# Kernel tuning notes

Measured on AMD Instinct MI355X. Metric: run time of the kernel, lower is better.

Reference implementation:

```python
import jax, jax.numpy as jnp
import numpy as np

TEMPERATURE = 0.07
BASE_TEMPERATURE = 0.07
L_MAX = 16  # max number of session labels per dialogue
NEG_INF = -1e30


def setup_inputs() -> dict:
    key = jax.random.key(0)
    k1, k2, k3 = jax.random.split(key, 3)
    B, T, H = 128, 1024, 256
    features = jax.random.normal(k1, (B, T, H), dtype=jnp.float32)
    dialogue_lengths = jax.random.randint(k2, (B,), 1, T + 1)
    labels = jax.random.randint(k3, (B, T), 0, L_MAX)
    return {"features": features, "dialogue_lengths": dialogue_lengths, "labels": labels}


def reference(features, dialogue_lengths, labels):
    B, T, H = features.shape
    valid = jnp.arange(T)[None, :] < dialogue_lengths[:, None]            # [B,T]
    # one-hot label assignment, zeroed at padded positions
    oh = (labels[..., None] == jnp.arange(L_MAX)[None, None, :]) & valid[..., None]
    ohf = oh.astype(features.dtype)                                       # [B,T,L]
    counts = ohf.sum(axis=1)                                              # [B,L]
    # per-dialogue, per-label prototype = mean of member features
    proto_sum = jnp.einsum('btl,bth->blh', ohf, features)                 # [B,L,H]
    prototypes = proto_sum / jnp.maximum(counts, 1.0)[..., None]          # [B,L,H]
    # anchor-vs-prototype logits
    logits = jnp.einsum('bth,blh->btl', features, prototypes) / TEMPERATURE
    present = counts > 0                                                  # [B,L]
    logits = jnp.where(present[:, None, :], logits, NEG_INF)
    log_prob = jax.nn.log_softmax(logits, axis=-1)                        # [B,T,L]
    # mask is one-hot on each token's own label -> mean_log_prob_pos is log_prob at own label
    pos = jnp.take_along_axis(log_prob, labels[..., None], axis=-1)[..., 0]  # [B,T]
    tok_loss = -(TEMPERATURE / BASE_TEMPERATURE) * pos
    per_dialogue = jnp.sum(jnp.where(valid, tok_loss, 0.0), axis=1) / dialogue_lengths.astype(features.dtype)
    return per_dialogue.mean()
```

## Files before the change

### kernel.cpp

```cpp
#include <hip/hip_runtime.h>
#include <math.h>

#define B 128
#define T 1024
#define H 256
#define L 16
#define INV_TEMP (1.0f/0.07f)
#define NEG_INF -1e30f


__global__ __launch_bounds__(256) void proto_kernel(
    const float* __restrict__ feat, const int* __restrict__ dlen,
    const int* __restrict__ labels, float* __restrict__ ws_pp,
    int* __restrict__ ws_cntp, float* __restrict__ out) {
  __shared__ int idx[L][256];
  __shared__ int cnt[L];

  const int bx = blockIdx.x;
  if (bx == 0 && threadIdx.x == 0) out[0] = 0.f;

  const int b = bx >> 4;
  const int seg = (bx >> 2) & 3;
  const int ch = bx & 3;
  const int tid = threadIdx.x;

  const int len = dlen[b];
  if (seg * 256 >= len) return;
  int segLen = len - seg * 256;
  if (segLen > 256) segLen = 256;

  if (tid < L) cnt[tid] = 0;
  __syncthreads();
  if (tid < segLen) {
    const int l = labels[(size_t)b * T + seg * 256 + tid];
    const int p = atomicAdd(&cnt[l], 1);
    idx[l][p] = tid;
  }
  __syncthreads();

  const int l = tid >> 4;
  const int cs = tid & 15;
  const float4* fb4 = (const float4*)feat +
      ((size_t)b * T + seg * 256) * (H / 4) + ch * 16 + cs;

  const int c = cnt[l];
  float4 a = make_float4(0.f, 0.f, 0.f, 0.f);
  int i = 0;
  for (; i + 8 <= c; i += 8) {
    int t8[8];
#pragma unroll
    for (int u = 0; u < 8; ++u) t8[u] = idx[l][i + u];
    float4 f8[8];
#pragma unroll
    for (int u = 0; u < 8; ++u) f8[u] = fb4[(size_t)t8[u] * (H / 4)];
#pragma unroll
    for (int u = 0; u < 8; ++u) {
      a.x += f8[u].x; a.y += f8[u].y; a.z += f8[u].z; a.w += f8[u].w;
    }
  }
  for (; i < c; ++i) {
    const float4 f = fb4[(size_t)idx[l][i] * (H / 4)];
    a.x += f.x; a.y += f.y; a.z += f.z; a.w += f.w;
  }

  *(float4*)(ws_pp + (((size_t)b * 4 + seg) * L + l) * H + ch * 64 + cs * 4) = a;
  if (ch == 0 && tid < L) ws_cntp[(b * 4 + seg) * L + tid] = cnt[tid];
}

__global__ __launch_bounds__(256) void dotsloss_kernel(
    const float* __restrict__ feat, const int* __restrict__ dlen,
    const int* __restrict__ labels, const float* __restrict__ ws_pp,
    const int* __restrict__ ws_cntp, float* __restrict__ out) {
  __shared__ float pr[L * H];
  __shared__ float part[256][L];
  __shared__ int cnts[L];
  __shared__ float red[256];

  const int b = blockIdx.x >> 2;
  const int q = blockIdx.x & 3;
  const int tid = threadIdx.x;

  const int len = dlen[b];
  if (q * 256 >= len) return;
  const int nseg = (len + 255) >> 8;

  if (tid < L) {
    const int* cp = ws_cntp + b * 4 * L + tid;
    int c = 0;
    for (int s = 0; s < nseg; ++s) c += cp[s * L];
    cnts[tid] = c;
  }
  __syncthreads();

  const float4* gp4 = (const float4*)(ws_pp + (size_t)b * 4 * L * H);
  for (int i = tid; i < L * H / 4; i += 256) {
    const int l = i >> 6;
    float4 s = gp4[i];
    for (int sg = 1; sg < nseg; ++sg) {
      const float4 t2 = gp4[sg * (L * 64) + i];
      s.x += t2.x; s.y += t2.y; s.z += t2.z; s.w += t2.w;
    }
    const int cn = cnts[l];
    const float inv = (cn > 0) ? 1.f / (float)cn : 0.f;
    ((float4*)pr)[i] = make_float4(s.x * inv, s.y * inv, s.z * inv, s.w * inv);
  }
  __syncthreads();

  const int ts = tid & 127;
  const int hh = tid >> 7;
  const int t0 = q * 256 + ts;
  const int t1 = t0 + 128;

  const float4* fA = (const float4*)feat + ((size_t)b * T + t0) * (H / 4) + hh * 32;
  const float4* fB = (const float4*)feat + ((size_t)b * T + t1) * (H / 4) + hh * 32;

  float dot0[L], dot1[L];
#pragma unroll
  for (int l = 0; l < L; ++l) { dot0[l] = 0.f; dot1[l] = 0.f; }

#pragma unroll 2
  for (int cb = 0; cb < 8; ++cb) {
    float4 fa[4], fb_[4];
#pragma unroll
    for (int q4 = 0; q4 < 4; ++q4) {
      fa[q4] = fA[cb * 4 + q4];
      fb_[q4] = fB[cb * 4 + q4];
    }
#pragma unroll
    for (int q4 = 0; q4 < 4; ++q4) {
#pragma unroll
      for (int l = 0; l < L; ++l) {
        const float4 p = *(const float4*)&pr[l * H + hh * 128 + cb * 16 + q4 * 4];
        dot0[l] += fa[q4].x * p.x + fa[q4].y * p.y +
                   fa[q4].z * p.z + fa[q4].w * p.w;
        dot1[l] += fb_[q4].x * p.x + fb_[q4].y * p.y +
                   fb_[q4].z * p.z + fb_[q4].w * p.w;
      }
    }
  }

  if (hh == 1) {
#pragma unroll
    for (int l = 0; l < L; ++l) {
      part[ts][l] = dot0[l];
      part[ts + 128][l] = dot1[l];
    }
  }
  __syncthreads();

  float tok = 0.f;
  if (hh == 0) {
#pragma unroll
    for (int k = 0; k < 2; ++k) {
      const int t = t0 + k * 128;
      if (t < len) {
        float lg[L];
#pragma unroll
        for (int l = 0; l < L; ++l) {
          const float d = (k == 0 ? dot0[l] : dot1[l]) + part[ts + k * 128][l];
          lg[l] = (cnts[l] > 0) ? d * INV_TEMP : NEG_INF;
        }
        float m = lg[0];
#pragma unroll
        for (int l = 1; l < L; ++l) m = fmaxf(m, lg[l]);
        float se = 0.f;
#pragma unroll
        for (int l = 0; l < L; ++l) se += expf(lg[l] - m);
        const float lsp = m + logf(se);

        const int lab = labels[(size_t)b * T + t];
        float pos = 0.f;
#pragma unroll
        for (int l = 0; l < L; ++l) pos += (l == lab) ? lg[l] : 0.f;

        tok += lsp - pos;
      }
    }
  }

  red[tid] = tok;
  __syncthreads();
#pragma unroll
  for (int s = 128; s > 0; s >>= 1) {
    if (tid < s) red[tid] += red[tid + s];
    __syncthreads();
  }
  if (tid == 0) atomicAdd(out, red[0] / ((float)len * (float)B));
}

extern "C" void kernel_launch(void* const* d_in, const int* in_sizes, int n_in,
                              void* d_out, int out_size, void* d_ws, size_t ws_size,
                              hipStream_t stream) {
  const float* feat = (const float*)d_in[0];
  const int* dlen = (const int*)d_in[1];
  const int* labels = (const int*)d_in[2];
  float* out = (float*)d_out;

  float* ws_pp = (float*)d_ws;
  int* ws_cntp = (int*)(ws_pp + (size_t)B * 4 * L * H);

  proto_kernel<<<B * 16, 256, 0, stream>>>(feat, dlen, labels, ws_pp,
                                           ws_cntp, out);
  dotsloss_kernel<<<B * 4, 256, 0, stream>>>(feat, dlen, labels, ws_pp,
                                             ws_cntp, out);
}
```

Baseline: 215.9 us.

## Compute full-dialogue prototypes in one block per channel chunk, drop segment reduction

The prototype kernel now assigns one block per (dialogue, channel quarter) covering all tokens instead of splitting into four 256-token segments, storing token indices as 16-bit in shared memory. Prototypes are normalized in place, so the loss kernel just copies them instead of summing partials and dividing. The shared-memory partial array also gets padding to avoid bank conflicts. This removes the partial-sum workspace traffic and reduction work, but cuts the proto grid to a quarter of the blocks, with longer serial gather loops per thread.

```diff
diff --git a/kernel.cpp b/kernel.cpp
--- a/kernel.cpp
+++ b/kernel.cpp
@@ -11,37 +11,32 @@
 
 __global__ __launch_bounds__(256) void proto_kernel(
     const float* __restrict__ feat, const int* __restrict__ dlen,
-    const int* __restrict__ labels, float* __restrict__ ws_pp,
-    int* __restrict__ ws_cntp, float* __restrict__ out) {
-  __shared__ int idx[L][256];
+    const int* __restrict__ labels, float* __restrict__ ws_proto,
+    int* __restrict__ ws_cnt, float* __restrict__ out) {
+  __shared__ unsigned short idx[L][T];
   __shared__ int cnt[L];
 
   const int bx = blockIdx.x;
   if (bx == 0 && threadIdx.x == 0) out[0] = 0.f;
 
-  const int b = bx >> 4;
-  const int seg = (bx >> 2) & 3;
+  const int b = bx >> 2;
   const int ch = bx & 3;
   const int tid = threadIdx.x;
-
   const int len = dlen[b];
-  if (seg * 256 >= len) return;
-  int segLen = len - seg * 256;
-  if (segLen > 256) segLen = 256;
 
   if (tid < L) cnt[tid] = 0;
   __syncthreads();
-  if (tid < segLen) {
-    const int l = labels[(size_t)b * T + seg * 256 + tid];
+  for (int t = tid; t < len; t += 256) {
+    const int l = labels[(size_t)b * T + t];
     const int p = atomicAdd(&cnt[l], 1);
-    idx[l][p] = tid;
+    idx[l][p] = (unsigned short)t;
   }
   __syncthreads();
 
   const int l = tid >> 4;
   const int cs = tid & 15;
   const float4* fb4 = (const float4*)feat +
-      ((size_t)b * T + seg * 256) * (H / 4) + ch * 16 + cs;
+      (size_t)b * T * (H / 4) + ch * 16 + cs;
 
   const int c = cnt[l];
   float4 a = make_float4(0.f, 0.f, 0.f, 0.f);
@@ -63,16 +58,18 @@
     a.x += f.x; a.y += f.y; a.z += f.z; a.w += f.w;
   }
 
-  *(float4*)(ws_pp + (((size_t)b * 4 + seg) * L + l) * H + ch * 64 + cs * 4) = a;
-  if (ch == 0 && tid < L) ws_cntp[(b * 4 + seg) * L + tid] = cnt[tid];
+  const float inv = (c > 0) ? 1.f / (float)c : 0.f;
+  a.x *= inv; a.y *= inv; a.z *= inv; a.w *= inv;
+  *(float4*)(ws_proto + ((size_t)b * L + l) * H + ch * 64 + cs * 4) = a;
+  if (ch == 0 && tid < L) ws_cnt[b * L + tid] = cnt[tid];
 }
 
 __global__ __launch_bounds__(256) void dotsloss_kernel(
     const float* __restrict__ feat, const int* __restrict__ dlen,
-    const int* __restrict__ labels, const float* __restrict__ ws_pp,
-    const int* __restrict__ ws_cntp, float* __restrict__ out) {
+    const int* __restrict__ labels, const float* __restrict__ ws_proto,
+    const int* __restrict__ ws_cnt, float* __restrict__ out) {
   __shared__ float pr[L * H];
-  __shared__ float part[256][L];
+  __shared__ float part[256][L + 1];
   __shared__ int cnts[L];
   __shared__ float red[256];
 
@@ -82,28 +79,12 @@
 
   const int len = dlen[b];
   if (q * 256 >= len) return;
-  const int nseg = (len + 255) >> 8;
 
-  if (tid < L) {
-    const int* cp = ws_cntp + b * 4 * L + tid;
-    int c = 0;
-    for (int s = 0; s < nseg; ++s) c += cp[s * L];
-    cnts[tid] = c;
-  }
+  if (tid < L) cnts[tid] = ws_cnt[b * L + tid];
   __syncthreads();
 
-  const float4* gp4 = (const float4*)(ws_pp + (size_t)b * 4 * L * H);
-  for (int i = tid; i < L * H / 4; i += 256) {
-    const int l = i >> 6;
-    float4 s = gp4[i];
-    for (int sg = 1; sg < nseg; ++sg) {
-      const float4 t2 = gp4[sg * (L * 64) + i];
-      s.x += t2.x; s.y += t2.y; s.z += t2.z; s.w += t2.w;
-    }
-    const int cn = cnts[l];
-    const float inv = (cn > 0) ? 1.f / (float)cn : 0.f;
-    ((float4*)pr)[i] = make_float4(s.x * inv, s.y * inv, s.z * inv, s.w * inv);
-  }
+  const float4* gp4 = (const float4*)(ws_proto + (size_t)b * L * H);
+  for (int i = tid; i < L * H / 4; i += 256) ((float4*)pr)[i] = gp4[i];
   __syncthreads();
 
   const int ts = tid & 127;
@@ -196,11 +177,11 @@
   const int* labels = (const int*)d_in[2];
   float* out = (float*)d_out;
 
-  float* ws_pp = (float*)d_ws;
-  int* ws_cntp = (int*)(ws_pp + (size_t)B * 4 * L * H);
+  float* ws_proto = (float*)d_ws;
+  int* ws_cnt = (int*)(ws_proto + (size_t)B * L * H);
 
-  proto_kernel<<<B * 16, 256, 0, stream>>>(feat, dlen, labels, ws_pp,
-                                           ws_cntp, out);
-  dotsloss_kernel<<<B * 4, 256, 0, stream>>>(feat, dlen, labels, ws_pp,
-                                             ws_cntp, out);
+  proto_kernel<<<B * 4, 256, 0, stream>>>(feat, dlen, labels, ws_proto,
+                                          ws_cnt, out);
+  dotsloss_kernel<<<B * 4, 256, 0, stream>>>(feat, dlen, labels, ws_proto,
+                                             ws_cnt, out);
 }
```

Result: no change. 213.7 us (-1.0%).
